# Kernel tuning notes

Measured on AMD Instinct MI355X. Metric: run time of the kernel, lower is better.

Reference implementation:

```python
import jax, jax.numpy as jnp
import numpy as np

_EPS = 1e-12  # torch F.normalize eps


def _normalize(x):
    # x: [B, N, 3]; matches torch.nn.functional.normalize(x, dim=2)
    norm = jnp.linalg.norm(x, axis=2, keepdims=True)
    return x / jnp.maximum(norm, _EPS)


def setup_inputs() -> dict:
    key = jax.random.key(0)
    k1, k2 = jax.random.split(key)
    xyz1 = jax.random.normal(k1, (8, 4096, 6), dtype=jnp.float32)
    xyz2 = jax.random.normal(k2, (8, 4096, 6), dtype=jnp.float32)
    return {"xyz1": xyz1, "xyz2": xyz2}


def reference(xyz1, xyz2):
    p1 = xyz1[:, :, :3]  # [B, N, 3]
    p2 = xyz2[:, :, :3]  # [B, M, 3]
    n1 = xyz1[:, :, 3:]  # [B, N, 3]
    n2 = xyz2[:, :, 3:]  # [B, M, 3]

    # Pairwise squared L2: |a|^2 + |b|^2 - 2 a.b  -> [B, N, M]
    sq1 = jnp.sum(p1 * p1, axis=2)  # [B, N]
    sq2 = jnp.sum(p2 * p2, axis=2)  # [B, M]
    cross = jnp.einsum('bnd,bmd->bnm', p1, p2)
    d = sq1[:, :, None] + sq2[:, None, :] - 2.0 * cross  # [B, N, M]

    dist1 = jnp.min(d, axis=2)      # [B, N] NN of each p1 in p2
    idx1 = jnp.argmin(d, axis=2)    # [B, N]
    dist2 = jnp.min(d, axis=1)      # [B, M] NN of each p2 in p1
    idx2 = jnp.argmin(d, axis=1)    # [B, M]

    # Gather matched normals
    t1 = jnp.take_along_axis(n2, idx1[:, :, None], axis=1)  # [B, N, 3]
    t2 = jnp.take_along_axis(n1, idx2[:, :, None], axis=1)  # [B, M, 3]

    nd1 = jnp.sum((_normalize(n1) - _normalize(t1)) ** 2, axis=2)  # [B, N]
    nd2 = jnp.sum((_normalize(n2) - _normalize(t2)) ** 2, axis=2)  # [B, M]

    return jnp.mean(dist1) + jnp.mean(dist2) + jnp.mean(nd1) + jnp.mean(nd2)
```

## Files before the change

kernel.cpp:

```cpp
#include <hip/hip_runtime.h>
#include <cstdint>

#define NB 8
#define NP 4096
#define THREADS 256
#define Q 4
#define CHUNK (THREADS * Q)
#define NCHUNK (NP / CHUNK)


template <int SEGV>
__global__ __launch_bounds__(THREADS) void chamfer_argmin(
    const float* __restrict__ xyz1, const float* __restrict__ xyz2,
    unsigned int* __restrict__ part)
{
    const int TSEG = NP / SEGV;
    __shared__ float4 tgt[NP / 16];

    unsigned int x = blockIdx.x;
    int seg   = x & (SEGV - 1);
    int chunk = (x / SEGV) & (NCHUNK - 1);
    int b     = (x / (SEGV * NCHUNK)) & 7;
    int dir   = x / (SEGV * NCHUNK * 8);

    const float* qset = dir ? xyz2 : xyz1;
    const float* tset = dir ? xyz1 : xyz2;

    int tbase = seg * TSEG;
    for (int t0 = threadIdx.x; t0 < TSEG; t0 += THREADS) {
        const float* src = tset + ((size_t)b * NP + tbase + t0) * 6;
        float tx = src[0], ty = src[1], tz = src[2];
        tgt[t0] = make_float4(tx, ty, tz, -0.5f * (tx * tx + ty * ty + tz * tz));
    }
    __syncthreads();

    float qx[Q], qy[Q], qz[Q], qq[Q], bs[Q];
    unsigned int bi[Q];
    int qbase = chunk * CHUNK + threadIdx.x;
    #pragma unroll
    for (int i = 0; i < Q; ++i) {
        const float* src = qset + ((size_t)b * NP + qbase + i * THREADS) * 6;
        qx[i] = src[0]; qy[i] = src[1]; qz[i] = src[2];
        qq[i] = qx[i] * qx[i] + qy[i] * qy[i] + qz[i] * qz[i];
        bs[i] = -3.4e38f;
        bi[i] = 0u;
    }

    #pragma unroll 4
    for (int k = 0; k < TSEG; ++k) {
        float4 t = tgt[k];
        unsigned int jb = (unsigned int)(tbase + k);
        #pragma unroll
        for (int i = 0; i < Q; ++i) {
            float s = fmaf(t.x, qx[i], fmaf(t.y, qy[i], fmaf(t.z, qz[i], t.w)));
            if (s > bs[i]) { bs[i] = s; bi[i] = jb; }
        }
    }

    unsigned int* slot =
        part + (((size_t)(dir * NB + b) * SEGV + seg) * NP) + qbase;
    #pragma unroll
    for (int i = 0; i < Q; ++i) {
        float d = fmaxf(fmaf(-2.0f, bs[i], qq[i]), 0.0f);
        slot[i * THREADS] = (__float_as_uint(d) & 0xFFFFF000u) | bi[i];
    }
}

template <int SEGV>
__global__ __launch_bounds__(256) void chamfer_finish(
    const float* __restrict__ xyz1, const float* __restrict__ xyz2,
    const unsigned int* __restrict__ part, float* __restrict__ out)
{
    int gid = blockIdx.x * 256 + threadIdx.x;
    int q   = gid & (NP - 1);
    int db  = gid >> 12;
    int b   = db & 7;
    int dir = db >> 3;

    const unsigned int* base = part + ((size_t)db * SEGV) * NP + q;
    unsigned int p = 0xFFFFFFFFu;
    #pragma unroll
    for (int s = 0; s < SEGV; ++s) p = min(p, base[(size_t)s * NP]);

    const float* qset = dir ? xyz2 : xyz1;
    const float* tset = dir ? xyz1 : xyz2;

    float dist = __uint_as_float(p & 0xFFFFF000u);
    int j = (int)(p & 0xFFFu);

    const float* nq = qset + ((size_t)b * NP + q) * 6 + 3;
    const float* nt = tset + ((size_t)b * NP + j) * 6 + 3;
    float ax = nq[0], ay = nq[1], az = nq[2];
    float bx = nt[0], by = nt[1], bz = nt[2];

    float na = fmaxf(sqrtf(ax * ax + ay * ay + az * az), 1e-12f);
    float nb = fmaxf(sqrtf(bx * bx + by * by + bz * bz), 1e-12f);
    float ra = 1.0f / na, rb = 1.0f / nb;
    float dx = ax * ra - bx * rb;
    float dy = ay * ra - by * rb;
    float dz = az * ra - bz * rb;
    float nd = dx * dx + dy * dy + dz * dz;

    float contrib = (dist + nd) * (1.0f / 32768.0f);

    for (int off = 32; off > 0; off >>= 1)
        contrib += __shfl_down(contrib, off, 64);
    __shared__ float wsum[4];
    if ((threadIdx.x & 63) == 0) wsum[threadIdx.x >> 6] = contrib;
    __syncthreads();
    if (threadIdx.x == 0)
        atomicAdd(out, wsum[0] + wsum[1] + wsum[2] + wsum[3]);
}

extern "C" void kernel_launch(void* const* d_in, const int* in_sizes, int n_in,
                              void* d_out, int out_size, void* d_ws, size_t ws_size,
                              hipStream_t stream) {
    const float* xyz1 = (const float*)d_in[0];
    const float* xyz2 = (const float*)d_in[1];
    float* out = (float*)d_out;
    unsigned int* part = (unsigned int*)d_ws;

    hipMemsetAsync(d_out, 0, sizeof(float), stream);

    size_t need32 = (size_t)2 * NB * 32 * NP * sizeof(unsigned int);
    if (ws_size >= need32) {
        chamfer_argmin<32><<<2 * NB * NCHUNK * 32, THREADS, 0, stream>>>(xyz1, xyz2, part);
        chamfer_finish<32><<<(2 * NB * NP) / 256, 256, 0, stream>>>(xyz1, xyz2, part, out);
    } else {
        chamfer_argmin<16><<<2 * NB * NCHUNK * 16, THREADS, 0, stream>>>(xyz1, xyz2, part);
        chamfer_finish<16><<<(2 * NB * NP) / 256, 256, 0, stream>>>(xyz1, xyz2, part, out);
    }
}
```

Baseline: 96.57 us.

## Compute pairwise distances with bf16x3-split MFMA and fused argmin epilogue

Replaces the scalar FMA nearest-neighbour search with MFMA bf16 matrix products, where each fp32 coordinate is split into three bf16 pieces so the dot products stay near fp32 accuracy. A prep kernel precomputes packed target tables and also zeroes the output. The main kernel streams targets into LDS via global_load_lds and reduces packed distance/index words with integer min. The normal-gather and mean epilogue is fused into the same kernel, removing the partial-result workspace and the separate finish pass. Risks: precision and tie-breaking differences in argmin, plus extra prep-kernel traffic.

```diff
diff --git a/kernel.cpp b/kernel.cpp
--- a/kernel.cpp
+++ b/kernel.cpp
@@ -3,113 +3,191 @@
 
 #define NB 8
 #define NP 4096
-#define THREADS 256
-#define Q 4
-#define CHUNK (THREADS * Q)
-#define NCHUNK (NP / CHUNK)
-
-
-template <int SEGV>
-__global__ __launch_bounds__(THREADS) void chamfer_argmin(
+
+typedef __attribute__((ext_vector_type(8))) short bf16x8;
+typedef __attribute__((ext_vector_type(4))) float f32x4;
+typedef __attribute__((ext_vector_type(4))) unsigned int u32x4;
+
+
+__device__ inline void split3(float x, unsigned short& a, unsigned short& b,
+                              unsigned short& c) {
+    unsigned int xb = __float_as_uint(x);
+    float s0 = __uint_as_float(xb & 0xFFFF0000u);
+    float r1 = x - s0;
+    unsigned int r1b = __float_as_uint(r1);
+    float s1 = __uint_as_float(r1b & 0xFFFF0000u);
+    float r2 = r1 - s1;
+    unsigned int r2b = __float_as_uint(r2);
+    a = (unsigned short)(xb >> 16);
+    b = (unsigned short)(r1b >> 16);
+    c = (unsigned short)(r2b >> 16);
+}
+
+__global__ __launch_bounds__(256) void chamfer_prep(
     const float* __restrict__ xyz1, const float* __restrict__ xyz2,
-    unsigned int* __restrict__ part)
+    unsigned int* __restrict__ atab, float* __restrict__ out)
 {
-    const int TSEG = NP / SEGV;
-    __shared__ float4 tgt[NP / 16];
-
-    unsigned int x = blockIdx.x;
-    int seg   = x & (SEGV - 1);
-    int chunk = (x / SEGV) & (NCHUNK - 1);
-    int b     = (x / (SEGV * NCHUNK)) & 7;
-    int dir   = x / (SEGV * NCHUNK * 8);
+    int gid = blockIdx.x * 256 + threadIdx.x;
+    if (gid == 0) out[0] = 0.0f;
+    int pt  = gid & (NP - 1);
+    int b   = (gid >> 12) & 7;
+    int set = gid >> 15;
+
+    const float* src = (set ? xyz2 : xyz1) + ((size_t)b * NP + pt) * 6;
+    float x = src[0], y = src[1], z = src[2];
+
+    unsigned short sx[3], sy[3], sz[3], sb[3];
+    split3(x, sx[0], sx[1], sx[2]);
+    split3(y, sy[0], sy[1], sy[2]);
+    split3(z, sz[0], sz[1], sz[2]);
+    float bias = 0.5f * (x * x + y * y + z * z);
+    split3(bias, sb[0], sb[1], sb[2]);
+
+    unsigned short S[32];
+    #pragma unroll
+    for (int d = 0; d < 3; ++d) {
+        #pragma unroll
+        for (int i = 0; i < 3; ++i) {
+            unsigned short v = (d == 0 ? sx[i] : (d == 1 ? sy[i] : sz[i]));
+            v ^= 0x8000;
+            #pragma unroll
+            for (int j = 0; j < 3; ++j) S[d * 9 + i * 3 + j] = v;
+        }
+    }
+    S[27] = sb[0]; S[28] = sb[1]; S[29] = sb[2];
+    S[30] = 0x3F80; S[31] = 0x3F80;
+
+    u32x4* dst = reinterpret_cast<u32x4*>(atab + (size_t)gid * 16);
+    #pragma unroll
+    for (int m = 0; m < 4; ++m) {
+        u32x4 w;
+        #pragma unroll
+        for (int e = 0; e < 4; ++e) {
+            int k = m * 8 + e * 2;
+            w[e] = (unsigned int)S[k] | ((unsigned int)S[k + 1] << 16);
+        }
+        dst[m] = w;
+    }
+}
+
+__device__ inline void gload_lds16(const unsigned int* g, unsigned int* l) {
+    __builtin_amdgcn_global_load_lds(
+        (const __attribute__((address_space(1))) unsigned int*)g,
+        (__attribute__((address_space(3))) unsigned int*)l, 16, 0, 0);
+}
+
+__global__ __launch_bounds__(256) void chamfer_mfma(
+    const float* __restrict__ xyz1, const float* __restrict__ xyz2,
+    const unsigned int* __restrict__ atab, float* __restrict__ out)
+{
+    __shared__ unsigned int stage[8192];
+    __shared__ unsigned int qbuf[4][16][16];
+    __shared__ float wredf[4];
+
+    int bx  = blockIdx.x;
+    int qc  = bx & 63;
+    int b   = (bx >> 6) & 7;
+    int dir = bx >> 9;
 
     const float* qset = dir ? xyz2 : xyz1;
     const float* tset = dir ? xyz1 : xyz2;
-
-    int tbase = seg * TSEG;
-    for (int t0 = threadIdx.x; t0 < TSEG; t0 += THREADS) {
-        const float* src = tset + ((size_t)b * NP + tbase + t0) * 6;
-        float tx = src[0], ty = src[1], tz = src[2];
-        tgt[t0] = make_float4(tx, ty, tz, -0.5f * (tx * tx + ty * ty + tz * tz));
+    int tid = threadIdx.x;
+    int w   = tid >> 6;
+    int l   = tid & 63;
+    int col = l & 15;
+    int g   = l >> 4;
+    int qbase = qc * 64 + w * 16;
+
+    if (l < 16) {
+        const float* qs = qset + ((size_t)b * NP + qbase + l) * 6;
+        float qx = qs[0], qy = qs[1], qz = qs[2];
+        unsigned short sx[3], sy[3], sz[3];
+        split3(qx, sx[0], sx[1], sx[2]);
+        split3(qy, sy[0], sy[1], sy[2]);
+        split3(qz, sz[0], sz[1], sz[2]);
+        float qq2 = 0.5f * (qx * qx + qy * qy + qz * qz);
+        unsigned int qqb = __float_as_uint(qq2);
+        float qh = __uint_as_float(qqb & 0xFFFF0000u);
+        unsigned int qlb = __float_as_uint(qq2 - qh);
+
+        unsigned short S[32];
+        #pragma unroll
+        for (int d = 0; d < 3; ++d)
+            #pragma unroll
+            for (int i = 0; i < 3; ++i)
+                #pragma unroll
+                for (int j = 0; j < 3; ++j)
+                    S[d * 9 + i * 3 + j] =
+                        (d == 0 ? sx[j] : (d == 1 ? sy[j] : sz[j]));
+        S[27] = 0x3F80; S[28] = 0x3F80; S[29] = 0x3F80;
+        S[30] = (unsigned short)(qqb >> 16);
+        S[31] = (unsigned short)(qlb >> 16);
+        #pragma unroll
+        for (int m = 0; m < 16; ++m)
+            qbuf[w][l][m] = (unsigned int)S[2 * m] | ((unsigned int)S[2 * m + 1] << 16);
     }
     __syncthreads();
-
-    float qx[Q], qy[Q], qz[Q], qq[Q], bs[Q];
-    unsigned int bi[Q];
-    int qbase = chunk * CHUNK + threadIdx.x;
+    bf16x8 bfrag = *reinterpret_cast<const bf16x8*>(&qbuf[w][col][g * 4]);
+
+    const unsigned int* atab_base =
+        atab + ((size_t)((1 - dir) * NB + b) * NP) * 16;
+
+    unsigned int p  = 0xFFFFFFFFu;
+    unsigned int vX = (unsigned int)(g * 4);
+    f32x4 czero = {0.0f, 0.0f, 0.0f, 0.0f};
+
+    for (int s0 = 0; s0 < NP; s0 += 512) {
+        const unsigned int* src = atab_base + (size_t)s0 * 16;
+        #pragma unroll
+        for (int r = 0; r < 8; ++r)
+            gload_lds16(src + r * 1024 + tid * 4, &stage[r * 1024 + tid * 4]);
+        __syncthreads();
+
+        #pragma unroll 4
+        for (int t = 0; t < 32; ++t) {
+            bf16x8 af = *reinterpret_cast<const bf16x8*>(
+                &stage[(t * 16 + col) * 16 + g * 4]);
+            f32x4 D = __builtin_amdgcn_mfma_f32_16x16x32_bf16(af, bfrag, czero, 0, 0, 0);
+            unsigned int p0 = (__float_as_uint(D[0]) & 0xFFFFF000u);
+            unsigned int p1 = (__float_as_uint(D[1]) & 0xFFFFF000u) | 1u;
+            unsigned int p2 = (__float_as_uint(D[2]) & 0xFFFFF000u) | 2u;
+            unsigned int p3 = (__float_as_uint(D[3]) & 0xFFFFF000u) | 3u;
+            unsigned int pm = min(min(p0, p1), min(p2, p3));
+            p = min(p, pm | vX);
+            vX += 16u;
+        }
+        __syncthreads();
+    }
+
+    p = min(p, (unsigned int)__shfl_xor((int)p, 16, 64));
+    p = min(p, (unsigned int)__shfl_xor((int)p, 32, 64));
+
+    float contrib = 0.0f;
+    if (l < 16) {
+        int q = qbase + l;
+        int idx = (int)(p & 0xFFFu);
+        float dist = fmaxf(2.0f * __uint_as_float(p & 0xFFFFF000u), 0.0f);
+
+        const float* nq = qset + ((size_t)b * NP + q) * 6 + 3;
+        const float* nt = tset + ((size_t)b * NP + idx) * 6 + 3;
+        float ax = nq[0], ay = nq[1], az = nq[2];
+        float bxn = nt[0], byn = nt[1], bzn = nt[2];
+        float na = fmaxf(sqrtf(ax * ax + ay * ay + az * az), 1e-12f);
+        float nb = fmaxf(sqrtf(bxn * bxn + byn * byn + bzn * bzn), 1e-12f);
+        float ra = 1.0f / na, rb = 1.0f / nb;
+        float dx = ax * ra - bxn * rb;
+        float dy = ay * ra - byn * rb;
+        float dz = az * ra - bzn * rb;
+        float nd = dx * dx + dy * dy + dz * dz;
+        contrib = (dist + nd) * (1.0f / 32768.0f);
+    }
     #pragma unroll
-    for (int i = 0; i < Q; ++i) {
-        const float* src = qset + ((size_t)b * NP + qbase + i * THREADS) * 6;
-        qx[i] = src[0]; qy[i] = src[1]; qz[i] = src[2];
-        qq[i] = qx[i] * qx[i] + qy[i] * qy[i] + qz[i] * qz[i];
-        bs[i] = -3.4e38f;
-        bi[i] = 0u;
-    }
-
-    #pragma unroll 4
-    for (int k = 0; k < TSEG; ++k) {
-        float4 t = tgt[k];
-        unsigned int jb = (unsigned int)(tbase + k);
-        #pragma unroll
-        for (int i = 0; i < Q; ++i) {
-            float s = fmaf(t.x, qx[i], fmaf(t.y, qy[i], fmaf(t.z, qz[i], t.w)));
-            if (s > bs[i]) { bs[i] = s; bi[i] = jb; }
-        }
-    }
-
-    unsigned int* slot =
-        part + (((size_t)(dir * NB + b) * SEGV + seg) * NP) + qbase;
-    #pragma unroll
-    for (int i = 0; i < Q; ++i) {
-        float d = fmaxf(fmaf(-2.0f, bs[i], qq[i]), 0.0f);
-        slot[i * THREADS] = (__float_as_uint(d) & 0xFFFFF000u) | bi[i];
-    }
-}
-
-template <int SEGV>
-__global__ __launch_bounds__(256) void chamfer_finish(
-    const float* __restrict__ xyz1, const float* __restrict__ xyz2,
-    const unsigned int* __restrict__ part, float* __restrict__ out)
-{
-    int gid = blockIdx.x * 256 + threadIdx.x;
-    int q   = gid & (NP - 1);
-    int db  = gid >> 12;
-    int b   = db & 7;
-    int dir = db >> 3;
-
-    const unsigned int* base = part + ((size_t)db * SEGV) * NP + q;
-    unsigned int p = 0xFFFFFFFFu;
-    #pragma unroll
-    for (int s = 0; s < SEGV; ++s) p = min(p, base[(size_t)s * NP]);
-
-    const float* qset = dir ? xyz2 : xyz1;
-    const float* tset = dir ? xyz1 : xyz2;
-
-    float dist = __uint_as_float(p & 0xFFFFF000u);
-    int j = (int)(p & 0xFFFu);
-
-    const float* nq = qset + ((size_t)b * NP + q) * 6 + 3;
-    const float* nt = tset + ((size_t)b * NP + j) * 6 + 3;
-    float ax = nq[0], ay = nq[1], az = nq[2];
-    float bx = nt[0], by = nt[1], bz = nt[2];
-
-    float na = fmaxf(sqrtf(ax * ax + ay * ay + az * az), 1e-12f);
-    float nb = fmaxf(sqrtf(bx * bx + by * by + bz * bz), 1e-12f);
-    float ra = 1.0f / na, rb = 1.0f / nb;
-    float dx = ax * ra - bx * rb;
-    float dy = ay * ra - by * rb;
-    float dz = az * ra - bz * rb;
-    float nd = dx * dx + dy * dy + dz * dz;
-
-    float contrib = (dist + nd) * (1.0f / 32768.0f);
-
-    for (int off = 32; off > 0; off >>= 1)
-        contrib += __shfl_down(contrib, off, 64);
-    __shared__ float wsum[4];
-    if ((threadIdx.x & 63) == 0) wsum[threadIdx.x >> 6] = contrib;
+    for (int off = 1; off < 64; off <<= 1)
+        contrib += __shfl_xor(contrib, off, 64);
+    if (l == 0) wredf[w] = contrib;
     __syncthreads();
-    if (threadIdx.x == 0)
-        atomicAdd(out, wsum[0] + wsum[1] + wsum[2] + wsum[3]);
+    if (tid == 0)
+        atomicAdd(out, wredf[0] + wredf[1] + wredf[2] + wredf[3]);
 }
 
 extern "C" void kernel_launch(void* const* d_in, const int* in_sizes, int n_in,
@@ -118,16 +196,8 @@
     const float* xyz1 = (const float*)d_in[0];
     const float* xyz2 = (const float*)d_in[1];
     float* out = (float*)d_out;
-    unsigned int* part = (unsigned int*)d_ws;
-
-    hipMemsetAsync(d_out, 0, sizeof(float), stream);
-
-    size_t need32 = (size_t)2 * NB * 32 * NP * sizeof(unsigned int);
-    if (ws_size >= need32) {
-        chamfer_argmin<32><<<2 * NB * NCHUNK * 32, THREADS, 0, stream>>>(xyz1, xyz2, part);
-        chamfer_finish<32><<<(2 * NB * NP) / 256, 256, 0, stream>>>(xyz1, xyz2, part, out);
-    } else {
-        chamfer_argmin<16><<<2 * NB * NCHUNK * 16, THREADS, 0, stream>>>(xyz1, xyz2, part);
-        chamfer_finish<16><<<(2 * NB * NP) / 256, 256, 0, stream>>>(xyz1, xyz2, part, out);
-    }
-}
+    unsigned int* atab = (unsigned int*)d_ws;
+
+    chamfer_prep<<<256, 256, 0, stream>>>(xyz1, xyz2, atab, out);
+    chamfer_mfma<<<1024, 256, 0, stream>>>(xyz1, xyz2, atab, out);
+}
```

Result: no change. 94.83 us (-1.8%).
